# Performance work log

Measured on AMD Instinct MI355X. Metric: run time of the kernel, lower is better.

The kernel has to match this reference:

```python
import jax, jax.numpy as jnp
import numpy as np

B, Q_LEN, HIDDEN, N_HEADS, HEAD_DIM = 8, 256, 4096, 32, 128
BLOCK_SIZE, BLOCKS_PER_SEQ, NUM_BLOCKS = 64, 12, 96
MAX_HIST = 512
ROPE_BASE = 10000.0


def setup_inputs() -> dict:
    key = jax.random.key(0)
    ks = jax.random.split(key, 8)
    hidden_states = jax.random.normal(ks[0], (1, B * Q_LEN, HIDDEN), jnp.float32)
    c_attn_w = jax.random.normal(ks[1], (3 * HIDDEN, HIDDEN), jnp.float32) * 0.02
    c_attn_b = jax.random.normal(ks[2], (3 * HIDDEN,), jnp.float32) * 0.02
    c_proj_w = jax.random.normal(ks[3], (HIDDEN, HIDDEN), jnp.float32) * 0.02
    k_cache = jax.random.normal(ks[4], (NUM_BLOCKS, BLOCK_SIZE, N_HEADS, HEAD_DIM), jnp.float32)
    v_cache = jax.random.normal(ks[5], (NUM_BLOCKS, BLOCK_SIZE, N_HEADS, HEAD_DIM), jnp.float32)
    history_lengths = jax.random.randint(ks[6], (B,), 0, MAX_HIST)
    block_offsets = jnp.arange(B * BLOCKS_PER_SEQ, dtype=jnp.int32).reshape(B, BLOCKS_PER_SEQ)
    return dict(hidden_states=hidden_states, c_attn_w=c_attn_w, c_attn_b=c_attn_b,
                c_proj_w=c_proj_w, k_cache=k_cache, v_cache=v_cache,
                history_lengths=history_lengths, block_offsets=block_offsets)


def _rotate_half(x):
    x1, x2 = x[..., :HEAD_DIM // 2], x[..., HEAD_DIM // 2:]
    return jnp.concatenate([-x2, x1], axis=-1)


def reference(hidden_states, c_attn_w, c_attn_b, c_proj_w, k_cache, v_cache,
              history_lengths, block_offsets):
    T = B * Q_LEN  # total tokens (continuous batching, flattened)
    x = hidden_states[0]  # [T, HIDDEN]
    # fused QKV projection
    qkv = x @ c_attn_w.T + c_attn_b  # [T, 3*HIDDEN]
    q, k, v = jnp.split(qkv, 3, axis=-1)
    q = q.reshape(T, N_HEADS, HEAD_DIM)
    k = k.reshape(T, N_HEADS, HEAD_DIM)
    v = v.reshape(T, N_HEADS, HEAD_DIM)
    # per-token absolute positions (position_ids_1d)
    positions = (history_lengths[:, None] + jnp.arange(Q_LEN)).reshape(-1)  # [T]
    # RoPE (ntk_alpha = 1)
    inv_freq = 1.0 / (ROPE_BASE ** (jnp.arange(0, HEAD_DIM, 2, dtype=jnp.float32) / HEAD_DIM))
    freqs = positions.astype(jnp.float32)[:, None] * inv_freq  # [T, D/2]
    emb = jnp.concatenate([freqs, freqs], axis=-1)  # [T, D]
    cos, sin = jnp.cos(emb)[:, None, :], jnp.sin(emb)[:, None, :]

    def rope(t):
        tf = t.astype(jnp.float32)
        return (tf * cos + _rotate_half(tf) * sin).astype(t.dtype)

    q, k = rope(q), rope(k)
    # fill_kv_cache: scatter new K/V into paged blocks at slot = position
    seq_ids = jnp.repeat(jnp.arange(B), Q_LEN)  # [T]
    blk = block_offsets[seq_ids, positions // BLOCK_SIZE]  # [T]
    slot = positions % BLOCK_SIZE  # [T]
    k_cache = k_cache.at[blk, slot].set(k)
    v_cache = v_cache.at[blk, slot].set(v)
    # paged attention: gather each sequence's blocks -> [B, KV, H, D]
    KV = BLOCKS_PER_SEQ * BLOCK_SIZE
    keys = k_cache[block_offsets].reshape(B, KV, N_HEADS, HEAD_DIM)
    vals = v_cache[block_offsets].reshape(B, KV, N_HEADS, HEAD_DIM)
    q_b = q.reshape(B, Q_LEN, N_HEADS, HEAD_DIM)
    scale = 1.0 / jnp.sqrt(jnp.asarray(HEAD_DIM, jnp.float32))
    scores = jnp.einsum('bqhd,bkhd->bhqk', q_b, keys) * scale  # [B,H,Q,KV]
    q_global = history_lengths[:, None] + jnp.arange(Q_LEN)  # [B,Q]
    causal = jnp.arange(KV)[None, None, :] <= q_global[:, :, None]  # [B,Q,KV]
    scores = jnp.where(causal[:, None, :, :], scores, jnp.finfo(scores.dtype).min)
    probs = jax.nn.softmax(scores, axis=-1)
    attn = jnp.einsum('bhqk,bkhd->bqhd', probs, vals).reshape(T, HIDDEN)
    out = attn @ c_proj_w.T  # c_proj (bias-free)
    return out.reshape(1, T, HIDDEN)
```

## Files before the change

### kernel.cpp

```cpp
#include <hip/hip_runtime.h>

typedef unsigned short ushort_t;
typedef float f32x4 __attribute__((ext_vector_type(4)));
typedef _Float16 f16x8 __attribute__((ext_vector_type(8)));
typedef short s16x8 __attribute__((ext_vector_type(8)));

#define NB 8
#define QL 256
#define HID 4096
#define NH 32
#define HD 128

__device__ __forceinline__ _Float16 f2h(float f) { return (_Float16)f; }
__device__ __forceinline__ ushort_t h2u(_Float16 h) {
  union { _Float16 h; ushort_t u; } x; x.h = h; return x.u;
}
__device__ __forceinline__ float u2f(ushort_t u) {
  union { _Float16 h; ushort_t u; } x; x.u = u; return (float)x.h;
}

#define MFMA16H(a, b, c) __builtin_amdgcn_mfma_f32_16x16x32_f16((a), (b), (c), 0, 0, 0)
#define AS1 __attribute__((address_space(1)))
#define AS3 __attribute__((address_space(3)))
#define VMCNT(n) asm volatile("s_waitcnt vmcnt(" #n ")" ::: "memory")
#define NOSTG

#define GLDS(srcp, dstofs)                                                    \
  __builtin_amdgcn_global_load_lds((const AS1 void*)(srcp),                   \
                                   (AS3 void*)&lds[dstofs], 16, 0, 0)

__global__ __launch_bounds__(256)
void conv_tile(const float* __restrict__ src, ushort_t* __restrict__ dst,
               int K, int ntiles) {
  const int tile = blockIdx.x * 4 + (threadIdx.x >> 6);
  if (tile >= ntiles) return;
  const int u = threadIdx.x & 63;
  const int row = u >> 2, seg = u & 3;
  const int K32 = K >> 5;
  const int mb = tile / K32, kb = tile % K32;
  const float* sp = src + (size_t)(mb * 16 + row) * K + kb * 32 + seg * 8;
  ushort_t t[8];
#pragma unroll
  for (int j = 0; j < 8; ++j) t[j] = h2u(f2h(sp[j]));
  *(s16x8*)(dst + (size_t)tile * 512 + (((seg << 4) | row) * 8)) = *(s16x8*)t;
}

template<int NT>
__global__ __launch_bounds__(512, 4)
void gemm_qkv(const ushort_t* __restrict__ At, const ushort_t* __restrict__ Bt,
              const float* __restrict__ bias, ushort_t* __restrict__ Ch,
              int N) {
  static_assert(NT % 3 == 2 && NT >= 8, "tail assumes NT%3==2");
  extern __shared__ ushort_t lds[];
  const int nwg = gridDim.x, bid = blockIdx.x;
  const int wg = (bid & 7) * (nwg >> 3) + (bid >> 3);
  const int mi = wg & 7, ni = wg >> 3;
  const int tid = threadIdx.x, w = tid >> 6, l = tid & 63;
  const int l16 = l & 15, lg = l >> 4;
  const int wm = w >> 1, wn = w & 1;

  const ushort_t* sA0 = At + ((size_t)(mi * 16 + 2 * w) * NT) * 512 + l * 8;
  const ushort_t* sA1 = At + ((size_t)(mi * 16 + 2 * w + 1) * NT) * 512 + l * 8;
  const ushort_t* sB  = Bt + ((size_t)(ni * 8 + w) * NT) * 512 + l * 8;

  int aof[4], bof[4];
#pragma unroll
  for (int mf = 0; mf < 4; ++mf) aof[mf] = (wm * 4 + mf) * 512 + l * 8;
#pragma unroll
  for (int nf = 0; nf < 4; ++nf) bof[nf] = 8192 + (wn * 4 + nf) * 512 + l * 8;

  f32x4 acc[4][4];
#pragma unroll
  for (int m = 0; m < 4; ++m)
#pragma unroll
    for (int n = 0; n < 4; ++n) acc[m][n] = (f32x4){0.f, 0.f, 0.f, 0.f};

#define STGQ(R, J)                                                            \
  do {                                                                        \
    GLDS(sA0 + (size_t)(J) * 512, (R) * 12288 + (2 * w) * 512);               \
    GLDS(sA1 + (size_t)(J) * 512, (R) * 12288 + (2 * w + 1) * 512);           \
    GLDS(sB + (size_t)(J) * 512, (R) * 12288 + 8192 + w * 512);               \
  } while (0)

#define ITERQ(R, VMW, STGCODE)                                                \
  do {                                                                        \
    VMW;                                                                      \
    __builtin_amdgcn_s_barrier();                                             \
    STGCODE;                                                                  \
    f16x8 fa[4], fb[4];                                                       \
    _Pragma("unroll") for (int mf = 0; mf < 4; ++mf)                          \
        fa[mf] = *(const f16x8*)&lds[(R) * 12288 + aof[mf]];                  \
    _Pragma("unroll") for (int nf = 0; nf < 4; ++nf)                          \
        fb[nf] = *(const f16x8*)&lds[(R) * 12288 + bof[nf]];                  \
    asm volatile("s_waitcnt lgkmcnt(0)" ::: "memory");                        \
    __builtin_amdgcn_sched_barrier(0);                                        \
    __builtin_amdgcn_s_setprio(1);                                            \
    _Pragma("unroll") for (int mf = 0; mf < 4; ++mf)                          \
    _Pragma("unroll") for (int nf = 0; nf < 4; ++nf)                          \
        acc[mf][nf] = MFMA16H(fa[mf], fb[nf], acc[mf][nf]);                   \
    __builtin_amdgcn_s_setprio(0);                                            \
  } while (0)

  STGQ(0, 0);
  STGQ(1, 1);
  for (int j = 0; j < NT - 2; j += 3) {
    ITERQ(0, VMCNT(3), STGQ(2, j + 2));
    ITERQ(1, VMCNT(3), STGQ(0, j + 3));
    ITERQ(2, VMCNT(3), STGQ(1, j + 4));
  }
  ITERQ(0, VMCNT(3), NOSTG);
  ITERQ(1, VMCNT(0), NOSTG);

#pragma unroll
  for (int nf = 0; nf < 4; ++nf) {
    const int col = ni * 128 + wn * 64 + nf * 16 + l16;
    const float bi = bias[col];
#pragma unroll
    for (int mf = 0; mf < 4; ++mf) {
      const int row0 = mi * 256 + wm * 64 + mf * 16 + lg * 4;
#pragma unroll
      for (int rr = 0; rr < 4; ++rr)
        Ch[(size_t)(row0 + rr) * N + col] = h2u(f2h(acc[mf][nf][rr] + bi));
    }
  }
#undef STGQ
#undef ITERQ
}

template<int NT>
__global__ __launch_bounds__(256, 3)
void gemm_proj(const ushort_t* __restrict__ At, const ushort_t* __restrict__ Bt,
               float* __restrict__ Cf, int N) {
  static_assert(NT % 3 == 2 && NT >= 8, "tail assumes NT%3==2");
  extern __shared__ ushort_t lds[];
  const int nwg = gridDim.x, bid = blockIdx.x;
  const int wg = (bid & 7) * (nwg >> 3) + (bid >> 3);
  const int mi = wg & 15, ni = wg >> 4;
  const int tid = threadIdx.x, w = tid >> 6, l = tid & 63;
  const int l16 = l & 15, lg = l >> 4;
  const int wm = w >> 1, wn = w & 1;

  const ushort_t* sA0 = At + ((size_t)(mi * 8 + 2 * w) * NT) * 512 + l * 8;
  const ushort_t* sA1 = At + ((size_t)(mi * 8 + 2 * w + 1) * NT) * 512 + l * 8;
  const ushort_t* sB0 = Bt + ((size_t)(ni * 8 + 2 * w) * NT) * 512 + l * 8;
  const ushort_t* sB1 = Bt + ((size_t)(ni * 8 + 2 * w + 1) * NT) * 512 + l * 8;

  int aof[4], bof[4];
#pragma unroll
  for (int mf = 0; mf < 4; ++mf) aof[mf] = (wm * 4 + mf) * 512 + l * 8;
#pragma unroll
  for (int nf = 0; nf < 4; ++nf) bof[nf] = 4096 + (wn * 4 + nf) * 512 + l * 8;

  f32x4 acc[4][4];
#pragma unroll
  for (int m = 0; m < 4; ++m)
#pragma unroll
    for (int n = 0; n < 4; ++n) acc[m][n] = (f32x4){0.f, 0.f, 0.f, 0.f};

#define STGP(R, J)                                                            \
  do {                                                                        \
    GLDS(sA0 + (size_t)(J) * 512, (R) * 8192 + (2 * w) * 512);                \
    GLDS(sA1 + (size_t)(J) * 512, (R) * 8192 + (2 * w + 1) * 512);            \
    GLDS(sB0 + (size_t)(J) * 512, (R) * 8192 + 4096 + (2 * w) * 512);         \
    GLDS(sB1 + (size_t)(J) * 512, (R) * 8192 + 4096 + (2 * w + 1) * 512);     \
  } while (0)

#define ITERP(R, VMW, STGCODE)                                                \
  do {                                                                        \
    VMW;                                                                      \
    __builtin_amdgcn_s_barrier();                                             \
    STGCODE;                                                                  \
    f16x8 fa[4], fb[4];                                                       \
    _Pragma("unroll") for (int mf = 0; mf < 4; ++mf)                          \
        fa[mf] = *(const f16x8*)&lds[(R) * 8192 + aof[mf]];                   \
    _Pragma("unroll") for (int nf = 0; nf < 4; ++nf)                          \
        fb[nf] = *(const f16x8*)&lds[(R) * 8192 + bof[nf]];                   \
    asm volatile("s_waitcnt lgkmcnt(0)" ::: "memory");                        \
    __builtin_amdgcn_sched_barrier(0);                                        \
    __builtin_amdgcn_s_setprio(1);                                            \
    _Pragma("unroll") for (int mf = 0; mf < 4; ++mf)                          \
    _Pragma("unroll") for (int nf = 0; nf < 4; ++nf)                          \
        acc[mf][nf] = MFMA16H(fa[mf], fb[nf], acc[mf][nf]);                   \
    __builtin_amdgcn_s_setprio(0);                                            \
  } while (0)

  STGP(0, 0);
  STGP(1, 1);
  for (int j = 0; j < NT - 2; j += 3) {
    ITERP(0, VMCNT(4), STGP(2, j + 2));
    ITERP(1, VMCNT(4), STGP(0, j + 3));
    ITERP(2, VMCNT(4), STGP(1, j + 4));
  }
  ITERP(0, VMCNT(4), NOSTG);
  ITERP(1, VMCNT(0), NOSTG);

#pragma unroll
  for (int nf = 0; nf < 4; ++nf) {
    const int col = ni * 128 + wn * 64 + nf * 16 + l16;
#pragma unroll
    for (int mf = 0; mf < 4; ++mf) {
      const int row0 = mi * 128 + wm * 64 + mf * 16 + lg * 4;
#pragma unroll
      for (int rr = 0; rr < 4; ++rr)
        Cf[(size_t)(row0 + rr) * N + col] = acc[mf][nf][rr];
    }
  }
#undef STGP
#undef ITERP
}

__global__ __launch_bounds__(256)
void rope_inplace(ushort_t* __restrict__ qkv, const int* __restrict__ hist) {
  const int t = blockIdx.x;
  const int b = t >> 8, qq = t & 255;
  __shared__ float cs[64], sn[64];
  const int tid = threadIdx.x;
  if (tid < 64) {
    const float pos = (float)(hist[b] + qq);
    const float f = pos * __expf(-(float)tid * (9.210340371976184f / 64.0f));
    cs[tid] = cosf(f);
    sn[tid] = sinf(f);
  }
  __syncthreads();
  ushort_t* row = qkv + (size_t)t * 12288;
  const int h = tid >> 3;
  const int j0 = (tid & 7) * 8;
  const float qscale = 0.08838834764831845f;
  float c[8], s[8];
#pragma unroll
  for (int j = 0; j < 8; ++j) { c[j] = cs[j0 + j]; s[j] = sn[j0 + j]; }
  {
    ushort_t* p1 = row + h * HD + j0;
    ushort_t* p2 = p1 + 64;
    s16x8 a = *(s16x8*)p1, bb = *(s16x8*)p2;
    ushort_t o1[8], o2[8];
#pragma unroll
    for (int j = 0; j < 8; ++j) {
      const float x1 = u2f((ushort_t)a[j]), x2 = u2f((ushort_t)bb[j]);
      o1[j] = h2u(f2h((x1 * c[j] - x2 * s[j]) * qscale));
      o2[j] = h2u(f2h((x2 * c[j] + x1 * s[j]) * qscale));
    }
    *(s16x8*)p1 = *(s16x8*)o1;
    *(s16x8*)p2 = *(s16x8*)o2;
  }
  {
    ushort_t* p1 = row + HID + h * HD + j0;
    ushort_t* p2 = p1 + 64;
    s16x8 a = *(s16x8*)p1, bb = *(s16x8*)p2;
    ushort_t o1[8], o2[8];
#pragma unroll
    for (int j = 0; j < 8; ++j) {
      const float x1 = u2f((ushort_t)a[j]), x2 = u2f((ushort_t)bb[j]);
      o1[j] = h2u(f2h(x1 * c[j] - x2 * s[j]));
      o2[j] = h2u(f2h(x2 * c[j] + x1 * s[j]));
    }
    *(s16x8*)p1 = *(s16x8*)o1;
    *(s16x8*)p2 = *(s16x8*)o2;
  }
}

__global__ __launch_bounds__(512, 2)
void attn_fwd(const ushort_t* __restrict__ qkv,
              const float* __restrict__ k_cache, const float* __restrict__ v_cache,
              const int* __restrict__ hist, const int* __restrict__ bofs,
              ushort_t* __restrict__ attn_t) {
  const int bh = blockIdx.x;
  const int b = bh >> 5, h = bh & 31;
  const int hb = hist[b];

  __shared__ ushort_t K_lds[64 * 136];
  __shared__ ushort_t V_lds[128 * 72];
  __shared__ ushort_t P_lds[256 * 72];

  const int tid = threadIdx.x;
  const int w = tid >> 6, l = tid & 63;
  const int l16 = l & 15, lg = l >> 4;

  f16x8 qf[2][4];
#pragma unroll
  for (int m = 0; m < 2; ++m) {
    const int qrow = w * 32 + m * 16 + l16;
    const ushort_t* qp = qkv + (size_t)(b * QL + qrow) * 12288 + h * HD + lg * 8;
#pragma unroll
    for (int kd = 0; kd < 4; ++kd) qf[m][kd] = *(const f16x8*)(qp + kd * 32);
  }

  f32x4 o[2][8];
  float mr[2][4], sr[2][4];
#pragma unroll
  for (int m = 0; m < 2; ++m) {
#pragma unroll
    for (int d = 0; d < 8; ++d) o[m][d] = (f32x4){0.f, 0.f, 0.f, 0.f};
#pragma unroll
    for (int r = 0; r < 4; ++r) { mr[m][r] = -1e30f; sr[m][r] = 0.f; }
  }

  const int nt = (hb + QL + 63) >> 6;
  const int srow = tid >> 4;
  const int seg = tid & 15;

  for (int t = 0; t < nt; ++t) {
    const int kv0 = t << 6;
    __syncthreads();
#pragma unroll
    for (int p = 0; p < 2; ++p) {
      const int row = p * 32 + srow;
      const int kvg = kv0 + row;
      if (kvg < hb) {
        const int blk = bofs[b * 12 + t];
        const size_t base = ((size_t)blk * 64 + (kvg & 63)) * HID + h * HD;
        const float* kf = k_cache + base;
        const float* vf = v_cache + base;
        ushort_t tmp[8];
#pragma unroll
        for (int j = 0; j < 8; ++j) tmp[j] = h2u(f2h(kf[seg * 8 + j]));
        *(s16x8*)&K_lds[row * 136 + seg * 8] = *(s16x8*)tmp;
#pragma unroll
        for (int j = 0; j < 8; ++j) {
          const int d = seg + j * 16;
          V_lds[d * 72 + row] = h2u(f2h(vf[d]));
        }
      } else {
        int r2 = kvg - hb;
        if (r2 > QL - 1) r2 = QL - 1;
        const size_t base = (size_t)(b * QL + r2) * 12288 + h * HD;
        const ushort_t* kb = qkv + base + HID;
        const ushort_t* vb = qkv + base + 2 * HID;
        *(s16x8*)&K_lds[row * 136 + seg * 8] = *(const s16x8*)(kb + seg * 8);
#pragma unroll
        for (int j = 0; j < 8; ++j) {
          const int d = seg + j * 16;
          V_lds[d * 72 + row] = vb[d];
        }
      }
    }
    __syncthreads();

    f32x4 sa[2][4];
#pragma unroll
    for (int m = 0; m < 2; ++m)
#pragma unroll
      for (int n = 0; n < 4; ++n) sa[m][n] = (f32x4){0.f, 0.f, 0.f, 0.f};
#pragma unroll
    for (int kd = 0; kd < 4; ++kd) {
      f16x8 kf[4];
#pragma unroll
      for (int n = 0; n < 4; ++n)
        kf[n] = *(const f16x8*)&K_lds[(n * 16 + l16) * 136 + kd * 32 + lg * 8];
#pragma unroll
      for (int m = 0; m < 2; ++m)
#pragma unroll
        for (int n = 0; n < 4; ++n)
          sa[m][n] = MFMA16H(qf[m][kd], kf[n], sa[m][n]);
    }

#pragma unroll
    for (int m = 0; m < 2; ++m) {
#pragma unroll
      for (int n = 0; n < 4; ++n) {
        const int kvg = kv0 + n * 16 + l16;
#pragma unroll
        for (int r = 0; r < 4; ++r) {
          const int qg = hb + w * 32 + m * 16 + lg * 4 + r;
          if (kvg > qg) sa[m][n][r] = -1e30f;
        }
      }
      float tm[4], ts[4];
#pragma unroll
      for (int r = 0; r < 4; ++r)
        tm[r] = fmaxf(fmaxf(sa[m][0][r], sa[m][1][r]),
                      fmaxf(sa[m][2][r], sa[m][3][r]));
#pragma unroll
      for (int x = 1; x < 16; x <<= 1)
#pragma unroll
        for (int r = 0; r < 4; ++r)
          tm[r] = fmaxf(tm[r], __shfl_xor(tm[r], x, 16));
#pragma unroll
      for (int r = 0; r < 4; ++r) {
        const float nm = fmaxf(mr[m][r], tm[r]);
        const float corr = __expf(mr[m][r] - nm);
        mr[m][r] = nm;
        sr[m][r] *= corr;
#pragma unroll
        for (int d = 0; d < 8; ++d) o[m][d][r] *= corr;
        ts[r] = 0.f;
      }
#pragma unroll
      for (int n = 0; n < 4; ++n)
#pragma unroll
        for (int r = 0; r < 4; ++r) {
          const float p = __expf(sa[m][n][r] - mr[m][r]);
          sa[m][n][r] = p;
          ts[r] += p;
        }
#pragma unroll
      for (int x = 1; x < 16; x <<= 1)
#pragma unroll
        for (int r = 0; r < 4; ++r) ts[r] += __shfl_xor(ts[r], x, 16);
#pragma unroll
      for (int r = 0; r < 4; ++r) sr[m][r] += ts[r];
#pragma unroll
      for (int n = 0; n < 4; ++n)
#pragma unroll
        for (int r = 0; r < 4; ++r)
          P_lds[(w * 32 + m * 16 + lg * 4 + r) * 72 + n * 16 + l16] =
              h2u(f2h(sa[m][n][r]));
    }

#pragma unroll
    for (int ks = 0; ks < 2; ++ks) {
      f16x8 pa[2];
#pragma unroll
      for (int m = 0; m < 2; ++m)
        pa[m] = *(const f16x8*)&P_lds[(w * 32 + m * 16 + l16) * 72 + ks * 32 + lg * 8];
#pragma unroll
      for (int d = 0; d < 8; ++d) {
        const f16x8 vb =
            *(const f16x8*)&V_lds[(d * 16 + l16) * 72 + ks * 32 + lg * 8];
#pragma unroll
        for (int m = 0; m < 2; ++m) o[m][d] = MFMA16H(pa[m], vb, o[m][d]);
      }
    }
  }

#pragma unroll
  for (int m = 0; m < 2; ++m) {
    const int rb = b * 16 + w * 2 + m;
#pragma unroll
    for (int r = 0; r < 4; ++r) {
      const float inv = 1.0f / sr[m][r];
#pragma unroll
      for (int d = 0; d < 8; ++d) {
        const int kb = h * 4 + (d >> 1);
        const int lane_dst = (lg * 4 + r) | ((((d & 1) << 1) | (l16 >> 3)) << 4);
        attn_t[((size_t)(rb * 128 + kb)) * 512 + lane_dst * 8 + (l16 & 7)] =
            h2u(f2h(o[m][d][r] * inv));
      }
    }
  }
}

extern "C" void kernel_launch(void* const* d_in, const int* in_sizes, int n_in,
                              void* d_out, int out_size, void* d_ws,
                              size_t ws_size, hipStream_t stream) {
  const float* hidden   = (const float*)d_in[0];
  const float* c_attn_w = (const float*)d_in[1];
  const float* c_attn_b = (const float*)d_in[2];
  const float* c_proj_w = (const float*)d_in[3];
  const float* k_cache  = (const float*)d_in[4];
  const float* v_cache  = (const float*)d_in[5];
  const int* hist       = (const int*)d_in[6];
  const int* bofs       = (const int*)d_in[7];
  float* out = (float*)d_out;

  char* ws = (char*)d_ws;
  const size_t MB = 1ull << 20;
  ushort_t* w_attn_t = (ushort_t*)(ws);
  ushort_t* wproj_t  = (ushort_t*)(ws);
  ushort_t* qkv_h   = (ushort_t*)(ws + 100 * MB);
  ushort_t* attn_t  = (ushort_t*)(ws + 148 * MB);
  ushort_t* x_t     = (ushort_t*)(ws + 196 * MB);

  conv_tile<<<4096, 256, 0, stream>>>(hidden, x_t, 4096, 16384);
  conv_tile<<<24576, 256, 0, stream>>>(c_attn_w, w_attn_t, 4096, 98304);
  gemm_qkv<128><<<768, 512, 73728, stream>>>(x_t, w_attn_t, c_attn_b, qkv_h,
                                             12288);
  rope_inplace<<<2048, 256, 0, stream>>>(qkv_h, hist);
  conv_tile<<<8192, 256, 0, stream>>>(c_proj_w, wproj_t, 4096, 32768);
  attn_fwd<<<256, 512, 0, stream>>>(qkv_h, k_cache, v_cache, hist, bofs,
                                    attn_t);
  gemm_proj<128><<<512, 256, 49152, stream>>>(attn_t, wproj_t, out, 4096);
}
```

Before: 407.8 us.

## Split attention query rows across two blocks per (batch, head)

The attention kernel now launches two workgroups per (batch, head), each handling 128 query rows with 16 rows per wave instead of 32. The upper-half workgroup iterates fewer KV tiles via a tighter causal bound, and the grid doubles from 256 to 512 blocks to better fill the GPU's compute units. In exchange, K/V tiles are loaded and converted twice (once per half), and each wave does less MFMA work per LDS load.

```diff
diff --git a/kernel.cpp b/kernel.cpp
--- a/kernel.cpp
+++ b/kernel.cpp
@@ -264,38 +264,35 @@
               const float* __restrict__ k_cache, const float* __restrict__ v_cache,
               const int* __restrict__ hist, const int* __restrict__ bofs,
               ushort_t* __restrict__ attn_t) {
-  const int bh = blockIdx.x;
+  const int bid = blockIdx.x;
+  const int qh = bid & 1, bh = bid >> 1;
   const int b = bh >> 5, h = bh & 31;
   const int hb = hist[b];
 
   __shared__ ushort_t K_lds[64 * 136];
   __shared__ ushort_t V_lds[128 * 72];
-  __shared__ ushort_t P_lds[256 * 72];
+  __shared__ ushort_t P_lds[128 * 72];
 
   const int tid = threadIdx.x;
   const int w = tid >> 6, l = tid & 63;
   const int l16 = l & 15, lg = l >> 4;
 
-  f16x8 qf[2][4];
-#pragma unroll
-  for (int m = 0; m < 2; ++m) {
-    const int qrow = w * 32 + m * 16 + l16;
+  f16x8 qf[4];
+  {
+    const int qrow = qh * 128 + w * 16 + l16;
     const ushort_t* qp = qkv + (size_t)(b * QL + qrow) * 12288 + h * HD + lg * 8;
 #pragma unroll
-    for (int kd = 0; kd < 4; ++kd) qf[m][kd] = *(const f16x8*)(qp + kd * 32);
-  }
-
-  f32x4 o[2][8];
-  float mr[2][4], sr[2][4];
-#pragma unroll
-  for (int m = 0; m < 2; ++m) {
-#pragma unroll
-    for (int d = 0; d < 8; ++d) o[m][d] = (f32x4){0.f, 0.f, 0.f, 0.f};
-#pragma unroll
-    for (int r = 0; r < 4; ++r) { mr[m][r] = -1e30f; sr[m][r] = 0.f; }
-  }
-
-  const int nt = (hb + QL + 63) >> 6;
+    for (int kd = 0; kd < 4; ++kd) qf[kd] = *(const f16x8*)(qp + kd * 32);
+  }
+
+  f32x4 o[8];
+  float mr[4], sr[4];
+#pragma unroll
+  for (int d = 0; d < 8; ++d) o[d] = (f32x4){0.f, 0.f, 0.f, 0.f};
+#pragma unroll
+  for (int r = 0; r < 4; ++r) { mr[r] = -1e30f; sr[r] = 0.f; }
+
+  const int nt = (hb + qh * 128 + 128 + 63) >> 6;
   const int srow = tid >> 4;
   const int seg = tid & 15;
 
@@ -336,11 +333,9 @@
     }
     __syncthreads();
 
-    f32x4 sa[2][4];
-#pragma unroll
-    for (int m = 0; m < 2; ++m)
-#pragma unroll
-      for (int n = 0; n < 4; ++n) sa[m][n] = (f32x4){0.f, 0.f, 0.f, 0.f};
+    f32x4 sa[4];
+#pragma unroll
+    for (int n = 0; n < 4; ++n) sa[n] = (f32x4){0.f, 0.f, 0.f, 0.f};
 #pragma unroll
     for (int kd = 0; kd < 4; ++kd) {
       f16x8 kf[4];
@@ -348,93 +343,80 @@
       for (int n = 0; n < 4; ++n)
         kf[n] = *(const f16x8*)&K_lds[(n * 16 + l16) * 136 + kd * 32 + lg * 8];
 #pragma unroll
-      for (int m = 0; m < 2; ++m)
-#pragma unroll
-        for (int n = 0; n < 4; ++n)
-          sa[m][n] = MFMA16H(qf[m][kd], kf[n], sa[m][n]);
-    }
-
-#pragma unroll
-    for (int m = 0; m < 2; ++m) {
-#pragma unroll
-      for (int n = 0; n < 4; ++n) {
-        const int kvg = kv0 + n * 16 + l16;
-#pragma unroll
-        for (int r = 0; r < 4; ++r) {
-          const int qg = hb + w * 32 + m * 16 + lg * 4 + r;
-          if (kvg > qg) sa[m][n][r] = -1e30f;
-        }
+      for (int n = 0; n < 4; ++n) sa[n] = MFMA16H(qf[kd], kf[n], sa[n]);
+    }
+
+#pragma unroll
+    for (int n = 0; n < 4; ++n) {
+      const int kvg = kv0 + n * 16 + l16;
+#pragma unroll
+      for (int r = 0; r < 4; ++r) {
+        const int qg = hb + qh * 128 + w * 16 + lg * 4 + r;
+        if (kvg > qg) sa[n][r] = -1e30f;
       }
-      float tm[4], ts[4];
+    }
+    float tm[4], ts[4];
+#pragma unroll
+    for (int r = 0; r < 4; ++r)
+      tm[r] = fmaxf(fmaxf(sa[0][r], sa[1][r]), fmaxf(sa[2][r], sa[3][r]));
+#pragma unroll
+    for (int x = 1; x < 16; x <<= 1)
+#pragma unroll
+      for (int r = 0; r < 4; ++r) tm[r] = fmaxf(tm[r], __shfl_xor(tm[r], x, 16));
+#pragma unroll
+    for (int r = 0; r < 4; ++r) {
+      const float nm = fmaxf(mr[r], tm[r]);
+      const float corr = __expf(mr[r] - nm);
+      mr[r] = nm;
+      sr[r] *= corr;
+#pragma unroll
+      for (int d = 0; d < 8; ++d) o[d][r] *= corr;
+      ts[r] = 0.f;
+    }
+#pragma unroll
+    for (int n = 0; n < 4; ++n)
+#pragma unroll
+      for (int r = 0; r < 4; ++r) {
+        const float p = __expf(sa[n][r] - mr[r]);
+        sa[n][r] = p;
+        ts[r] += p;
+      }
+#pragma unroll
+    for (int x = 1; x < 16; x <<= 1)
+#pragma unroll
+      for (int r = 0; r < 4; ++r) ts[r] += __shfl_xor(ts[r], x, 16);
+#pragma unroll
+    for (int r = 0; r < 4; ++r) sr[r] += ts[r];
+#pragma unroll
+    for (int n = 0; n < 4; ++n)
 #pragma unroll
       for (int r = 0; r < 4; ++r)
-        tm[r] = fmaxf(fmaxf(sa[m][0][r], sa[m][1][r]),
-                      fmaxf(sa[m][2][r], sa[m][3][r]));
-#pragma unroll
-      for (int x = 1; x < 16; x <<= 1)
-#pragma unroll
-        for (int r = 0; r < 4; ++r)
-          tm[r] = fmaxf(tm[r], __shfl_xor(tm[r], x, 16));
-#pragma unroll
-      for (int r = 0; r < 4; ++r) {
-        const float nm = fmaxf(mr[m][r], tm[r]);
-        const float corr = __expf(mr[m][r] - nm);
-        mr[m][r] = nm;
-        sr[m][r] *= corr;
-#pragma unroll
-        for (int d = 0; d < 8; ++d) o[m][d][r] *= corr;
-        ts[r] = 0.f;
-      }
-#pragma unroll
-      for (int n = 0; n < 4; ++n)
-#pragma unroll
-        for (int r = 0; r < 4; ++r) {
-          const float p = __expf(sa[m][n][r] - mr[m][r]);
-          sa[m][n][r] = p;
-          ts[r] += p;
-        }
-#pragma unroll
-      for (int x = 1; x < 16; x <<= 1)
-#pragma unroll
-        for (int r = 0; r < 4; ++r) ts[r] += __shfl_xor(ts[r], x, 16);
-#pragma unroll
-      for (int r = 0; r < 4; ++r) sr[m][r] += ts[r];
-#pragma unroll
-      for (int n = 0; n < 4; ++n)
-#pragma unroll
-        for (int r = 0; r < 4; ++r)
-          P_lds[(w * 32 + m * 16 + lg * 4 + r) * 72 + n * 16 + l16] =
-              h2u(f2h(sa[m][n][r]));
-    }
+        P_lds[(w * 16 + lg * 4 + r) * 72 + n * 16 + l16] = h2u(f2h(sa[n][r]));
 
 #pragma unroll
     for (int ks = 0; ks < 2; ++ks) {
-      f16x8 pa[2];
-#pragma unroll
-      for (int m = 0; m < 2; ++m)
-        pa[m] = *(const f16x8*)&P_lds[(w * 32 + m * 16 + l16) * 72 + ks * 32 + lg * 8];
+      const f16x8 pa =
+          *(const f16x8*)&P_lds[(w * 16 + l16) * 72 + ks * 32 + lg * 8];
 #pragma unroll
       for (int d = 0; d < 8; ++d) {
         const f16x8 vb =
             *(const f16x8*)&V_lds[(d * 16 + l16) * 72 + ks * 32 + lg * 8];
-#pragma unroll
-        for (int m = 0; m < 2; ++m) o[m][d] = MFMA16H(pa[m], vb, o[m][d]);
+        o[d] = MFMA16H(pa, vb, o[d]);
       }
     }
   }
 
-#pragma unroll
-  for (int m = 0; m < 2; ++m) {
-    const int rb = b * 16 + w * 2 + m;
+  {
+    const int rb = b * 16 + qh * 8 + w;
 #pragma unroll
     for (int r = 0; r < 4; ++r) {
-      const float inv = 1.0f / sr[m][r];
+      const float inv = 1.0f / sr[r];
 #pragma unroll
       for (int d = 0; d < 8; ++d) {
         const int kb = h * 4 + (d >> 1);
         const int lane_dst = (lg * 4 + r) | ((((d & 1) << 1) | (l16 >> 3)) << 4);
         attn_t[((size_t)(rb * 128 + kb)) * 512 + lane_dst * 8 + (l16 & 7)] =
-            h2u(f2h(o[m][d][r] * inv));
+            h2u(f2h(o[d][r] * inv));
       }
     }
   }
@@ -467,7 +449,7 @@
                                              12288);
   rope_inplace<<<2048, 256, 0, stream>>>(qkv_h, hist);
   conv_tile<<<8192, 256, 0, stream>>>(c_proj_w, wproj_t, 4096, 32768);
-  attn_fwd<<<256, 512, 0, stream>>>(qkv_h, k_cache, v_cache, hist, bofs,
+  attn_fwd<<<512, 512, 0, stream>>>(qkv_h, k_cache, v_cache, hist, bofs,
                                     attn_t);
   gemm_proj<128><<<512, 256, 49152, stream>>>(attn_t, wproj_t, out, 4096);
 }
```

New measurement: 419.2 us. 2.8% more time.
